# Kernel optimization log

Measured on AMD Instinct MI355X. Metric: run time of the kernel, lower is better.

## Reference

```python
import jax, jax.numpy as jnp
import numpy as np

E = 768   # embedding_dim
D = 64    # head_dim
B = 8
S = 2048


def setup_inputs() -> dict:
    key = jax.random.key(0)
    k1, k2, k3, k4 = jax.random.split(key, 4)
    inputs = jax.random.normal(k1, (B, S, E), dtype=jnp.float32)
    # causal mask: 1 where attending allowed, 0 elsewhere (masked_fill where ==0)
    attention_mask = jnp.tril(jnp.ones((S, S), dtype=jnp.int32))[None, :, :]
    Q = jax.random.normal(k2, (E, D), dtype=jnp.float32) * 0.01
    K = jax.random.normal(k3, (E, D), dtype=jnp.float32) * 0.01
    V = jax.random.normal(k4, (E, D), dtype=jnp.float32) * 0.01
    return {"inputs": inputs, "attention_mask": attention_mask, "Q": Q, "K": K, "V": V}


def reference(inputs, attention_mask, Q, K, V):
    scale = 1.0 / np.sqrt(D).astype(np.float32)
    q = inputs @ Q          # [B,S,D]
    k = inputs @ K          # [B,S,D]
    v = inputs @ V          # [B,S,D]
    w = jnp.einsum('bqd,bkd->bqk', q, k) * scale   # [B,S,S]
    w = jnp.where(attention_mask == 0, -jnp.inf, w)
    attn = jax.nn.softmax(w, axis=-1)              # [B,S,S]
    states = attn @ v                              # [B,S,D] (dropout p=0.0 is identity)
    return states
```

## Files before the change

### kernel.cpp

```cpp
#include <hip/hip_runtime.h>
#include <cstdint>

#define B_ 8
#define S_ 2048
#define E_ 768
#define D_ 64
#define NSPLIT 4
#define SEGLEN (S_ / NSPLIT)
#define ROWS (B_ * S_)

typedef unsigned short ushort_t;
typedef __attribute__((ext_vector_type(8))) short s16x8;
typedef __attribute__((ext_vector_type(4))) float f32x4;

__device__ inline ushort_t f2bf(float f) {
  unsigned int x = __float_as_uint(f);
  return (ushort_t)((x + 0x7fffu + ((x >> 16) & 1u)) >> 16);
}

__device__ inline unsigned int pkbf(float hi, float lo) {
  return __builtin_amdgcn_perm(__float_as_uint(hi) + 0x8000u,
                               __float_as_uint(lo) + 0x8000u, 0x07060302u);
}

__device__ inline void async16(const void* g, void* l) {
  __builtin_amdgcn_global_load_lds(
      (const __attribute__((address_space(1))) unsigned int*)g,
      (__attribute__((address_space(3))) unsigned int*)l, 16, 0, 0);
}

__global__ __launch_bounds__(256) void wt_kernel(
    const float* __restrict__ Wq, const float* __restrict__ Wk,
    const float* __restrict__ Wv, ushort_t* __restrict__ wt) {
  const int mat = blockIdx.y;
  const int e = blockIdx.x * 4 + (threadIdx.x >> 6);
  const int d = threadIdx.x & 63;
  const float* W = (mat == 0) ? Wq : ((mat == 1) ? Wk : Wv);
  wt[(long)(mat * 64 + d) * E_ + e] = f2bf(W[(long)e * D_ + d]);
}

__global__ __launch_bounds__(256) void qkv_mfma(
    const float* __restrict__ in, const ushort_t* __restrict__ wt,
    ushort_t* __restrict__ qb, ushort_t* __restrict__ kb,
    ushort_t* __restrict__ vtb) {
  const int tid = threadIdx.x;
  const int w = tid >> 6;
  const int L = tid & 63;
  const int c = L & 15;
  const int q = L >> 4;
  const int row0 = blockIdx.x * 32;

  __shared__ float Alds[2][32][64];
  __shared__ ushort_t Blds[2][192][64];

  const int ar0 = w * 8 + (L >> 4);
  const int ar1 = ar0 + 4;
  const int asl = L & 15;
  const float* asrc0 = in + (long)(row0 + ar0) * E_ + ((asl ^ (ar0 & 15)) << 2);
  const float* asrc1 = in + (long)(row0 + ar1) * E_ + ((asl ^ (ar1 & 15)) << 2);
  const int bsl = L & 7;
  const ushort_t* bsrc[6];
#pragma unroll
  for (int jj = 0; jj < 6; ++jj) {
    const int br = w * 48 + jj * 8 + (L >> 3);
    bsrc[jj] = wt + (long)br * E_ + ((bsl ^ (br & 7)) << 3);
  }
  float* ad[2] = {&Alds[0][w * 8][0], &Alds[1][w * 8][0]};
  ushort_t* bd[2] = {&Blds[0][w * 48][0], &Blds[1][w * 48][0]};

  const int mloc = w & 1;
  const int nbase = (w >> 1) * 6;
  const int ra = mloc * 16 + c;
  const int offA00 = ra * 256 + ((2 * q + 0) ^ c) * 16;
  const int offA01 = ra * 256 + ((2 * q + 1) ^ c) * 16;
  const int offA10 = ra * 256 + ((8 + 2 * q + 0) ^ c) * 16;
  const int offA11 = ra * 256 + ((8 + 2 * q + 1) ^ c) * 16;
  int offB0[6], offB1[6];
#pragma unroll
  for (int t = 0; t < 6; ++t) {
    const int n = (nbase + t) * 16 + c;
    offB0[t] = n * 128 + ((q + 0) ^ (c & 7)) * 16;
    offB1[t] = n * 128 + ((q + 4) ^ (c & 7)) * 16;
  }
  const char* Abase = (const char*)&Alds[0][0][0];
  const char* Bbase = (const char*)&Blds[0][0][0];

  f32x4 acc[6];
#pragma unroll
  for (int n = 0; n < 6; ++n) acc[n] = (f32x4){0.f, 0.f, 0.f, 0.f};

  async16(asrc0, ad[0]);
  async16(asrc1, ad[0] + 4 * 64);
#pragma unroll
  for (int jj = 0; jj < 6; ++jj) async16(bsrc[jj], bd[0] + jj * 8 * 64);
  asrc0 += 64; asrc1 += 64;
#pragma unroll
  for (int jj = 0; jj < 6; ++jj) bsrc[jj] += 64;

  for (int it = 0; it < E_ / 64; ++it) {
    const int b = it & 1;
    __syncthreads();
    if (it + 1 < E_ / 64) {
      const int nb = 1 - b;
      async16(asrc0, ad[nb]);
      async16(asrc1, ad[nb] + 4 * 64);
#pragma unroll
      for (int jj = 0; jj < 6; ++jj) async16(bsrc[jj], bd[nb] + jj * 8 * 64);
      asrc0 += 64; asrc1 += 64;
#pragma unroll
      for (int jj = 0; jj < 6; ++jj) bsrc[jj] += 64;
    }
    const char* Ab = Abase + b * 8192;
    const char* Bb = Bbase + b * 24576;
    const float4 a00 = *(const float4*)(Ab + offA00);
    const float4 a01 = *(const float4*)(Ab + offA01);
    const float4 a10 = *(const float4*)(Ab + offA10);
    const float4 a11 = *(const float4*)(Ab + offA11);
    union { s16x8 v; unsigned int u[4]; } af0, af1;
    af0.u[0] = pkbf(a00.y, a00.x);
    af0.u[1] = pkbf(a00.w, a00.z);
    af0.u[2] = pkbf(a01.y, a01.x);
    af0.u[3] = pkbf(a01.w, a01.z);
    af1.u[0] = pkbf(a10.y, a10.x);
    af1.u[1] = pkbf(a10.w, a10.z);
    af1.u[2] = pkbf(a11.y, a11.x);
    af1.u[3] = pkbf(a11.w, a11.z);
#pragma unroll
    for (int t = 0; t < 6; ++t) {
      const s16x8 bf0 = *(const s16x8*)(Bb + offB0[t]);
      const s16x8 bf1 = *(const s16x8*)(Bb + offB1[t]);
      acc[t] = __builtin_amdgcn_mfma_f32_16x16x32_bf16(af0.v, bf0, acc[t], 0, 0, 0);
      acc[t] = __builtin_amdgcn_mfma_f32_16x16x32_bf16(af1.v, bf1, acc[t], 0, 0, 0);
    }
  }

  const float qscale = 0.125f * 1.44269504088896340736f;
  const int row0w = row0 + mloc * 16;
  const int b_ = row0w >> 11;
  const int srow = row0w & (S_ - 1);
#pragma unroll
  for (int n = 0; n < 6; ++n) {
    const int gn = nbase + n;
    const int mat = gn >> 2;
    const int d0 = (gn & 3) * 16 + c;
#pragma unroll
    for (int reg = 0; reg < 4; ++reg) {
      const int m = q * 4 + reg;
      const float x = acc[n][reg];
      if (mat == 0) {
        qb[(long)(row0w + m) * D_ + d0] = f2bf(x * qscale);
      } else if (mat == 1) {
        kb[(long)(row0w + m) * D_ + d0] = f2bf(x);
      } else {
        vtb[(long)b_ * D_ * S_ + (long)d0 * S_ + srow + m] = f2bf(x);
      }
    }
  }
}

__global__ __launch_bounds__(256) void attn_mfma(
    const ushort_t* __restrict__ qb, const ushort_t* __restrict__ kb,
    const ushort_t* __restrict__ vtb, float* __restrict__ op,
    float* __restrict__ lw) {
  const int qb0 = blockIdx.x * 64;
  const int batch = blockIdx.y;
  const int seg = blockIdx.z;
  const int j0 = seg * SEGLEN;
  const int jmax = min(j0 + SEGLEN, qb0 + 64);
  if (j0 >= jmax) return;
  const int ntiles = (jmax - j0) >> 6;

  const int w = threadIdx.x >> 6;
  const int L = threadIdx.x & 63;
  const int col = L & 15;
  const int quad = L >> 4;

  __shared__ ushort_t Kl[2][64][64];
  __shared__ ushort_t Vl[2][64][64];
  __shared__ ushort_t Pl[4][16][72];

  const ushort_t* kbb = kb + (long)batch * S_ * D_;
  const ushort_t* vbb = vtb + (long)batch * D_ * S_;

  const int rl = (w << 4) + (L >> 3);
  const int gsw = (L & 7) ^ (rl & 7);
  const ushort_t* ksrc = kbb + ((long)(j0 + rl) << 6) + gsw * 8;
  const ushort_t* vsrc = vbb + (long)rl * S_ + j0 + gsw * 8;
  ushort_t* kdst[2] = {&Kl[0][w * 16][0], &Kl[1][w * 16][0]};
  ushort_t* vdst[2] = {&Vl[0][w * 16][0], &Vl[1][w * 16][0]};

  const int s0 = ((quad ^ (col & 7)) * 16);

  const ushort_t* qrow = qb + ((long)(batch * S_ + qb0 + w * 16 + col) * D_);
  const s16x8 qf0 = *(const s16x8*)(qrow + quad * 8);
  const s16x8 qf1 = *(const s16x8*)(qrow + 32 + quad * 8);

  f32x4 O[4];
#pragma unroll
  for (int t = 0; t < 4; ++t) O[t] = (f32x4){0.f, 0.f, 0.f, 0.f};
  float l[4] = {0.f, 0.f, 0.f, 0.f};

  async16(ksrc, kdst[0]);
  async16(ksrc + 512, kdst[0] + 512);
  async16(vsrc, vdst[0]);
  async16(vsrc + 8 * S_, vdst[0] + 512);
  ksrc += 64 * 64; vsrc += 64;

  for (int i = 0; i < ntiles; ++i) {
    const int b = i & 1;
    const int kt = j0 + i * 64;
    __syncthreads();
    if (i + 1 < ntiles) {
      const int nb = 1 - b;
      async16(ksrc, kdst[nb]);
      async16(ksrc + 512, kdst[nb] + 512);
      async16(vsrc, vdst[nb]);
      async16(vsrc + 8 * S_, vdst[nb] + 512);
      ksrc += 64 * 64; vsrc += 64;
    }
    const char* Kb = (const char*)&Kl[b][0][0];
    const char* Vb = (const char*)&Vl[b][0][0];

    f32x4 S[4];
#pragma unroll
    for (int t = 0; t < 4; ++t) {
      const s16x8 kf0 = *(const s16x8*)(Kb + (t * 16 + col) * 128 + s0);
      const s16x8 kf1 = *(const s16x8*)(Kb + (t * 16 + col) * 128 + (s0 ^ 64));
      f32x4 z = (f32x4){0.f, 0.f, 0.f, 0.f};
      z = __builtin_amdgcn_mfma_f32_16x16x32_bf16(qf0, kf0, z, 0, 0, 0);
      S[t] = __builtin_amdgcn_mfma_f32_16x16x32_bf16(qf1, kf1, z, 0, 0, 0);
    }
    if (kt + 64 > qb0) {
#pragma unroll
      for (int t = 0; t < 4; ++t) {
        const int colg = kt + t * 16 + col;
#pragma unroll
        for (int reg = 0; reg < 4; ++reg) {
          const int rowg = qb0 + w * 16 + quad * 4 + reg;
          if (colg > rowg) S[t][reg] = -1e30f;
        }
      }
    }
    float P[4][4];
#pragma unroll
    for (int t = 0; t < 4; ++t)
#pragma unroll
      for (int reg = 0; reg < 4; ++reg) {
        P[t][reg] = exp2f(S[t][reg]);
        l[reg] += P[t][reg];
      }
#pragma unroll
    for (int t = 0; t < 4; ++t)
#pragma unroll
      for (int reg = 0; reg < 4; ++reg)
        Pl[w][quad * 4 + reg][t * 16 + col] = f2bf(P[t][reg]);
    const s16x8 p0 = *(const s16x8*)&Pl[w][col][quad * 8];
    const s16x8 p1 = *(const s16x8*)&Pl[w][col][32 + quad * 8];
#pragma unroll
    for (int t = 0; t < 4; ++t) {
      const s16x8 vf0 = *(const s16x8*)(Vb + (t * 16 + col) * 128 + s0);
      const s16x8 vf1 = *(const s16x8*)(Vb + (t * 16 + col) * 128 + (s0 ^ 64));
      O[t] = __builtin_amdgcn_mfma_f32_16x16x32_bf16(p0, vf0, O[t], 0, 0, 0);
      O[t] = __builtin_amdgcn_mfma_f32_16x16x32_bf16(p1, vf1, O[t], 0, 0, 0);
    }
  }
#pragma unroll
  for (int off = 1; off < 16; off <<= 1)
#pragma unroll
    for (int reg = 0; reg < 4; ++reg)
      l[reg] += __shfl_xor(l[reg], off);

  const int growbase = batch * S_ + qb0 + w * 16;
#pragma unroll
  for (int t = 0; t < 4; ++t)
#pragma unroll
    for (int reg = 0; reg < 4; ++reg)
      op[((long)seg * ROWS + growbase + quad * 4 + reg) * D_ + t * 16 + col] =
          O[t][reg];
  if (col == 0) {
#pragma unroll
    for (int reg = 0; reg < 4; ++reg)
      lw[(long)seg * ROWS + growbase + quad * 4 + reg] = l[reg];
  }
}

__global__ __launch_bounds__(256) void attn_combine(
    const float* __restrict__ op, const float* __restrict__ lw,
    float* __restrict__ out) {
  const int t = threadIdx.x;
  const int d = t & 63;
  const int g = blockIdx.x * 4 + (t >> 6);
  const int s_q = g & (S_ - 1);
  float osum = 0.f, lsum = 0.f;
#pragma unroll
  for (int s = 0; s < NSPLIT; ++s) {
    if (s_q >= s * SEGLEN) {
      osum += op[((long)s * ROWS + g) * D_ + d];
      lsum += lw[(long)s * ROWS + g];
    }
  }
  out[(long)g * D_ + d] = osum / lsum;
}

extern "C" void kernel_launch(void* const* d_in, const int* in_sizes, int n_in,
                              void* d_out, int out_size, void* d_ws, size_t ws_size,
                              hipStream_t stream) {
  const float* in = (const float*)d_in[0];
  const float* Wq = (const float*)d_in[2];
  const float* Wk = (const float*)d_in[3];
  const float* Wv = (const float*)d_in[4];
  float* out = (float*)d_out;

  ushort_t* qbuf = (ushort_t*)d_ws;
  ushort_t* kbuf = qbuf + (long)ROWS * D_;
  ushort_t* vtb = kbuf + (long)ROWS * D_;
  float* op = (float*)(vtb + (long)ROWS * D_);
  float* lw = op + (long)NSPLIT * ROWS * D_;
  ushort_t* wt = (ushort_t*)(lw + (long)NSPLIT * ROWS);

  wt_kernel<<<dim3(E_ / 4, 3), 256, 0, stream>>>(Wq, Wk, Wv, wt);
  qkv_mfma<<<ROWS / 32, 256, 0, stream>>>(in, wt, qbuf, kbuf, vtb);
  attn_mfma<<<dim3(S_ / 64, B_, NSPLIT), 256, 0, stream>>>(qbuf, kbuf, vtb, op, lw);
  attn_combine<<<(ROWS * D_) / 256, 256, 0, stream>>>(op, lw, out);
}
```

Baseline: 140.2 us.

## Split attention into one block per causal tile pair with atomic accumulation

Replaces the 4-way sequence split, where each block loops over its key tiles, with a triangular grid that launches one block per (query tile, key tile) pair. Each block computes its partial P·V and row sums and adds them into global accumulators with float atomics, then a normalize kernel divides. A zero kernel is added to clear the accumulators. The aim is better load balance across the causal triangle. The cost is heavy atomic traffic (every tile pair does 64x64 atomic adds), repeated Q loads, and no cross-tile pipelining of the K/V loads.

After: 181.8 us. +29.7%, slower.

```diff
diff --git a/kernel.cpp b/kernel.cpp
--- a/kernel.cpp
+++ b/kernel.cpp
@@ -5,9 +5,8 @@
 #define S_ 2048
 #define E_ 768
 #define D_ 64
-#define NSPLIT 4
-#define SEGLEN (S_ / NSPLIT)
 #define ROWS (B_ * S_)
+#define NTILES 528
 
 typedef unsigned short ushort_t;
 typedef __attribute__((ext_vector_type(8))) short s16x8;
@@ -27,6 +26,12 @@
   __builtin_amdgcn_global_load_lds(
       (const __attribute__((address_space(1))) unsigned int*)g,
       (__attribute__((address_space(3))) unsigned int*)l, 16, 0, 0);
+}
+
+__global__ __launch_bounds__(256) void zero_kernel(float* __restrict__ p,
+                                                   int n4) {
+  const int i = blockIdx.x * 256 + threadIdx.x;
+  if (i < n4) ((float4*)p)[i] = make_float4(0.f, 0.f, 0.f, 0.f);
 }
 
 __global__ __launch_bounds__(256) void wt_kernel(
@@ -158,111 +163,96 @@
   }
 }
 
-__global__ __launch_bounds__(256) void attn_mfma(
-    const ushort_t* __restrict__ qb, const ushort_t* __restrict__ kb,
-    const ushort_t* __restrict__ vtb, float* __restrict__ op,
-    float* __restrict__ lw) {
-  const int qb0 = blockIdx.x * 64;
+__global__ __launch_bounds__(256) void attn_tile(
+    const ushort_t* __restrict__ qbuf, const ushort_t* __restrict__ kb,
+    const ushort_t* __restrict__ vtb, float* __restrict__ Oacc,
+    float* __restrict__ lacc) {
+  const int x = blockIdx.x;
+  int qb = (int)((sqrtf(8.f * (float)x + 1.f) - 1.f) * 0.5f);
+  while ((qb + 1) * (qb + 2) / 2 <= x) ++qb;
+  while (qb * (qb + 1) / 2 > x) --qb;
+  const int t64 = x - qb * (qb + 1) / 2;
   const int batch = blockIdx.y;
-  const int seg = blockIdx.z;
-  const int j0 = seg * SEGLEN;
-  const int jmax = min(j0 + SEGLEN, qb0 + 64);
-  if (j0 >= jmax) return;
-  const int ntiles = (jmax - j0) >> 6;
+  const int qb0 = qb * 64;
+  const int kt = t64 * 64;
 
   const int w = threadIdx.x >> 6;
   const int L = threadIdx.x & 63;
   const int col = L & 15;
   const int quad = L >> 4;
 
-  __shared__ ushort_t Kl[2][64][64];
-  __shared__ ushort_t Vl[2][64][64];
+  __shared__ ushort_t Kl[64][64];
+  __shared__ ushort_t Vl[64][64];
   __shared__ ushort_t Pl[4][16][72];
 
   const ushort_t* kbb = kb + (long)batch * S_ * D_;
   const ushort_t* vbb = vtb + (long)batch * D_ * S_;
 
   const int rl = (w << 4) + (L >> 3);
-  const int gsw = (L & 7) ^ (rl & 7);
-  const ushort_t* ksrc = kbb + ((long)(j0 + rl) << 6) + gsw * 8;
-  const ushort_t* vsrc = vbb + (long)rl * S_ + j0 + gsw * 8;
-  ushort_t* kdst[2] = {&Kl[0][w * 16][0], &Kl[1][w * 16][0]};
-  ushort_t* vdst[2] = {&Vl[0][w * 16][0], &Vl[1][w * 16][0]};
-
-  const int s0 = ((quad ^ (col & 7)) * 16);
-
-  const ushort_t* qrow = qb + ((long)(batch * S_ + qb0 + w * 16 + col) * D_);
+  const int gsw = (L & 7) ^ (L >> 3);
+  const ushort_t* ksrc = kbb + ((long)(kt + rl) << 6) + gsw * 8;
+  const ushort_t* vsrc = vbb + (long)rl * S_ + kt + gsw * 8;
+  async16(ksrc, &Kl[w * 16][0]);
+  async16(ksrc + 512, &Kl[w * 16][0] + 512);
+  async16(vsrc, &Vl[w * 16][0]);
+  async16(vsrc + 8 * S_, &Vl[w * 16][0] + 512);
+
+  const ushort_t* qrow = qbuf + ((long)(batch * S_ + qb0 + w * 16 + col) * D_);
   const s16x8 qf0 = *(const s16x8*)(qrow + quad * 8);
   const s16x8 qf1 = *(const s16x8*)(qrow + 32 + quad * 8);
 
+  const int s0 = ((quad ^ (col & 7)) * 16);
+
+  __syncthreads();
+
+  f32x4 S[4];
+#pragma unroll
+  for (int t = 0; t < 4; ++t) {
+    const s16x8 kf0 = *(const s16x8*)((const char*)&Kl[0][0] +
+                                      (t * 16 + col) * 128 + s0);
+    const s16x8 kf1 = *(const s16x8*)((const char*)&Kl[0][0] +
+                                      (t * 16 + col) * 128 + (s0 ^ 64));
+    f32x4 z = (f32x4){0.f, 0.f, 0.f, 0.f};
+    z = __builtin_amdgcn_mfma_f32_16x16x32_bf16(qf0, kf0, z, 0, 0, 0);
+    S[t] = __builtin_amdgcn_mfma_f32_16x16x32_bf16(qf1, kf1, z, 0, 0, 0);
+  }
+  if (t64 == qb) {
+#pragma unroll
+    for (int t = 0; t < 4; ++t) {
+      const int colg = kt + t * 16 + col;
+#pragma unroll
+      for (int reg = 0; reg < 4; ++reg) {
+        const int rowg = qb0 + w * 16 + quad * 4 + reg;
+        if (colg > rowg) S[t][reg] = -1e30f;
+      }
+    }
+  }
+  float P[4][4];
+  float l[4] = {0.f, 0.f, 0.f, 0.f};
+#pragma unroll
+  for (int t = 0; t < 4; ++t)
+#pragma unroll
+    for (int reg = 0; reg < 4; ++reg) {
+      P[t][reg] = exp2f(S[t][reg]);
+      l[reg] += P[t][reg];
+    }
+#pragma unroll
+  for (int t = 0; t < 4; ++t)
+#pragma unroll
+    for (int reg = 0; reg < 4; ++reg)
+      Pl[w][quad * 4 + reg][t * 16 + col] = f2bf(P[t][reg]);
+  const s16x8 p0 = *(const s16x8*)&Pl[w][col][quad * 8];
+  const s16x8 p1 = *(const s16x8*)&Pl[w][col][32 + quad * 8];
   f32x4 O[4];
 #pragma unroll
-  for (int t = 0; t < 4; ++t) O[t] = (f32x4){0.f, 0.f, 0.f, 0.f};
-  float l[4] = {0.f, 0.f, 0.f, 0.f};
-
-  async16(ksrc, kdst[0]);
-  async16(ksrc + 512, kdst[0] + 512);
-  async16(vsrc, vdst[0]);
-  async16(vsrc + 8 * S_, vdst[0] + 512);
-  ksrc += 64 * 64; vsrc += 64;
-
-  for (int i = 0; i < ntiles; ++i) {
-    const int b = i & 1;
-    const int kt = j0 + i * 64;
-    __syncthreads();
-    if (i + 1 < ntiles) {
-      const int nb = 1 - b;
-      async16(ksrc, kdst[nb]);
-      async16(ksrc + 512, kdst[nb] + 512);
-      async16(vsrc, vdst[nb]);
-      async16(vsrc + 8 * S_, vdst[nb] + 512);
-      ksrc += 64 * 64; vsrc += 64;
-    }
-    const char* Kb = (const char*)&Kl[b][0][0];
-    const char* Vb = (const char*)&Vl[b][0][0];
-
-    f32x4 S[4];
-#pragma unroll
-    for (int t = 0; t < 4; ++t) {
-      const s16x8 kf0 = *(const s16x8*)(Kb + (t * 16 + col) * 128 + s0);
-      const s16x8 kf1 = *(const s16x8*)(Kb + (t * 16 + col) * 128 + (s0 ^ 64));
-      f32x4 z = (f32x4){0.f, 0.f, 0.f, 0.f};
-      z = __builtin_amdgcn_mfma_f32_16x16x32_bf16(qf0, kf0, z, 0, 0, 0);
-      S[t] = __builtin_amdgcn_mfma_f32_16x16x32_bf16(qf1, kf1, z, 0, 0, 0);
-    }
-    if (kt + 64 > qb0) {
-#pragma unroll
-      for (int t = 0; t < 4; ++t) {
-        const int colg = kt + t * 16 + col;
-#pragma unroll
-        for (int reg = 0; reg < 4; ++reg) {
-          const int rowg = qb0 + w * 16 + quad * 4 + reg;
-          if (colg > rowg) S[t][reg] = -1e30f;
-        }
-      }
-    }
-    float P[4][4];
-#pragma unroll
-    for (int t = 0; t < 4; ++t)
-#pragma unroll
-      for (int reg = 0; reg < 4; ++reg) {
-        P[t][reg] = exp2f(S[t][reg]);
-        l[reg] += P[t][reg];
-      }
-#pragma unroll
-    for (int t = 0; t < 4; ++t)
-#pragma unroll
-      for (int reg = 0; reg < 4; ++reg)
-        Pl[w][quad * 4 + reg][t * 16 + col] = f2bf(P[t][reg]);
-    const s16x8 p0 = *(const s16x8*)&Pl[w][col][quad * 8];
-    const s16x8 p1 = *(const s16x8*)&Pl[w][col][32 + quad * 8];
-#pragma unroll
-    for (int t = 0; t < 4; ++t) {
-      const s16x8 vf0 = *(const s16x8*)(Vb + (t * 16 + col) * 128 + s0);
-      const s16x8 vf1 = *(const s16x8*)(Vb + (t * 16 + col) * 128 + (s0 ^ 64));
-      O[t] = __builtin_amdgcn_mfma_f32_16x16x32_bf16(p0, vf0, O[t], 0, 0, 0);
-      O[t] = __builtin_amdgcn_mfma_f32_16x16x32_bf16(p1, vf1, O[t], 0, 0, 0);
-    }
+  for (int t = 0; t < 4; ++t) {
+    const s16x8 vf0 = *(const s16x8*)((const char*)&Vl[0][0] +
+                                      (t * 16 + col) * 128 + s0);
+    const s16x8 vf1 = *(const s16x8*)((const char*)&Vl[0][0] +
+                                      (t * 16 + col) * 128 + (s0 ^ 64));
+    f32x4 z = (f32x4){0.f, 0.f, 0.f, 0.f};
+    z = __builtin_amdgcn_mfma_f32_16x16x32_bf16(p0, vf0, z, 0, 0, 0);
+    O[t] = __builtin_amdgcn_mfma_f32_16x16x32_bf16(p1, vf1, z, 0, 0, 0);
   }
 #pragma unroll
   for (int off = 1; off < 16; off <<= 1)
@@ -270,36 +260,27 @@
     for (int reg = 0; reg < 4; ++reg)
       l[reg] += __shfl_xor(l[reg], off);
 
-  const int growbase = batch * S_ + qb0 + w * 16;
+  const long growbase = (long)batch * S_ + qb0 + w * 16;
 #pragma unroll
   for (int t = 0; t < 4; ++t)
 #pragma unroll
     for (int reg = 0; reg < 4; ++reg)
-      op[((long)seg * ROWS + growbase + quad * 4 + reg) * D_ + t * 16 + col] =
-          O[t][reg];
+      atomicAdd(&Oacc[(growbase + quad * 4 + reg) * D_ + t * 16 + col],
+                O[t][reg]);
   if (col == 0) {
 #pragma unroll
     for (int reg = 0; reg < 4; ++reg)
-      lw[(long)seg * ROWS + growbase + quad * 4 + reg] = l[reg];
-  }
-}
-
-__global__ __launch_bounds__(256) void attn_combine(
-    const float* __restrict__ op, const float* __restrict__ lw,
+      atomicAdd(&lacc[growbase + quad * 4 + reg], l[reg]);
+  }
+}
+
+__global__ __launch_bounds__(256) void attn_norm(
+    const float* __restrict__ Oacc, const float* __restrict__ lacc,
     float* __restrict__ out) {
   const int t = threadIdx.x;
   const int d = t & 63;
   const int g = blockIdx.x * 4 + (t >> 6);
-  const int s_q = g & (S_ - 1);
-  float osum = 0.f, lsum = 0.f;
-#pragma unroll
-  for (int s = 0; s < NSPLIT; ++s) {
-    if (s_q >= s * SEGLEN) {
-      osum += op[((long)s * ROWS + g) * D_ + d];
-      lsum += lw[(long)s * ROWS + g];
-    }
-  }
-  out[(long)g * D_ + d] = osum / lsum;
+  out[(long)g * D_ + d] = Oacc[(long)g * D_ + d] / lacc[g];
 }
 
 extern "C" void kernel_launch(void* const* d_in, const int* in_sizes, int n_in,
@@ -314,12 +295,14 @@
   ushort_t* qbuf = (ushort_t*)d_ws;
   ushort_t* kbuf = qbuf + (long)ROWS * D_;
   ushort_t* vtb = kbuf + (long)ROWS * D_;
-  float* op = (float*)(vtb + (long)ROWS * D_);
-  float* lw = op + (long)NSPLIT * ROWS * D_;
-  ushort_t* wt = (ushort_t*)(lw + (long)NSPLIT * ROWS);
-
+  float* Oacc = (float*)(vtb + (long)ROWS * D_);
+  float* lacc = Oacc + (long)ROWS * D_;
+  ushort_t* wt = (ushort_t*)(lacc + ROWS);
+
+  const int n4 = (ROWS * D_ + ROWS) / 4;
+  zero_kernel<<<(n4 + 255) / 256, 256, 0, stream>>>(Oacc, n4);
   wt_kernel<<<dim3(E_ / 4, 3), 256, 0, stream>>>(Wq, Wk, Wv, wt);
   qkv_mfma<<<ROWS / 32, 256, 0, stream>>>(in, wt, qbuf, kbuf, vtb);
-  attn_mfma<<<dim3(S_ / 64, B_, NSPLIT), 256, 0, stream>>>(qbuf, kbuf, vtb, op, lw);
-  attn_combine<<<(ROWS * D_) / 256, 256, 0, stream>>>(op, lw, out);
-}
+  attn_tile<<<dim3(NTILES, B_), 256, 0, stream>>>(qbuf, kbuf, vtb, Oacc, lacc);
+  attn_norm<<<(ROWS * D_) / 256, 256, 0, stream>>>(Oacc, lacc, out);
+}
```
